# Kernel optimization log

Hardware: AMD Instinct MI355X
Metric: run time of the kernel (lower is better)

The kernel has to match this reference:

```python
import jax, jax.numpy as jnp
import numpy as np

MIN_NORM = 1e-15
BALL_EPS = 1e-5  # fp32 boundary eps used by hgcn PoincareBall.proj
C_IN = 1.0       # curvature = 1/r_in^2, r_in = 1.0
C_OUT = 1.0      # curvature = 1/r_out^2, r_out = 1.0


def _artanh(x):
    # hgcn clamps to +/-(1-1e-15); use 1e-7 so fp32 does not round to exactly 1
    x = jnp.clip(x, -1.0 + 1e-7, 1.0 - 1e-7)
    return 0.5 * (jnp.log1p(x) - jnp.log1p(-x))


def _norm(x):
    return jnp.maximum(jnp.linalg.norm(x, axis=-1, keepdims=True), MIN_NORM)


def proj(x, c):
    norm = _norm(x)
    maxnorm = (1.0 - BALL_EPS) / jnp.sqrt(c)
    return jnp.where(norm > maxnorm, x / norm * maxnorm, x)


def expmap0(u, c):
    sc = jnp.sqrt(c)
    un = _norm(u)
    return jnp.tanh(sc * un) * u / (sc * un)


def logmap0(p, c):
    sc = jnp.sqrt(c)
    pn = _norm(p)
    return _artanh(sc * pn) * p / (sc * pn)


def mobius_matvec(m, x, c):
    sc = jnp.sqrt(c)
    xn = _norm(x)
    mx = x @ m.T                      # [N, out]
    mxn = _norm(mx)
    res = jnp.tanh(mxn / xn * _artanh(sc * xn)) * mx / (mxn * sc)
    zero_row = jnp.all(mx == 0, axis=-1, keepdims=True)
    return jnp.where(zero_row, jnp.zeros((), dtype=res.dtype), res)


def mobius_add(x, y, c):
    x2 = jnp.sum(x * x, axis=-1, keepdims=True)
    y2 = jnp.sum(y * y, axis=-1, keepdims=True)
    xy = jnp.sum(x * y, axis=-1, keepdims=True)
    num = (1.0 + 2.0 * c * xy + c * y2) * x + (1.0 - c * x2) * y
    denom = 1.0 + 2.0 * c * xy + c * c * x2 * y2
    return num / jnp.maximum(denom, MIN_NORM)


def setup_inputs() -> dict:
    key = jax.random.key(0)
    k1, k2, k3, k4 = jax.random.split(key, 4)
    N, D_IN, D_OUT = 8192, 256, 256
    # points on the ball: small tangent vectors mapped through proj
    x = proj(0.05 * jax.random.normal(k1, (N, D_IN), dtype=jnp.float32), C_IN)
    # dense row-normalized adjacency
    adj = jax.random.uniform(k2, (N, N), dtype=jnp.float32)
    adj = adj / jnp.sum(adj, axis=1, keepdims=True)
    # xavier_uniform with gain sqrt(2)
    bound = np.sqrt(2.0) * np.sqrt(6.0 / (D_IN + D_OUT))
    weight = jax.random.uniform(k3, (D_OUT, D_IN), dtype=jnp.float32,
                                minval=-bound, maxval=bound)
    bias = 0.01 * jax.random.normal(k4, (D_OUT,), dtype=jnp.float32)
    return {"x": x, "adj": adj, "weight": weight, "bias": bias}


def reference(x, adj, weight, bias):
    # --- HypLinear (dropout=0 in eval) ---
    h = proj(mobius_matvec(weight, x, C_IN), C_IN)
    hyp_bias = proj(expmap0(bias[None, :], C_IN), C_IN)  # proj_tan0 = identity
    h = proj(mobius_add(h, hyp_bias, C_IN), C_IN)
    # --- HypAgg (use_att=False): aggregate in tangent space at origin ---
    x_tangent = logmap0(h, C_IN)
    support_t = adj @ x_tangent                          # [N, out]
    h = proj(expmap0(support_t, C_IN), C_IN)
    # --- HypAct: relu in tangent space, re-embed with c_out ---
    xt = jax.nn.relu(logmap0(h, C_IN))                   # proj_tan0 = identity
    return proj(expmap0(xt, C_OUT), C_OUT)
```

## Files before the change

kernel.cpp:

```cpp
#include <hip/hip_runtime.h>
#include <stdint.h>

#define DIM 256
#define NROWS 8192
#define KTOT 8192

typedef unsigned short u16;
typedef short bf16x8 __attribute__((ext_vector_type(8)));
typedef float f32x4 __attribute__((ext_vector_type(4)));

__device__ __forceinline__ u16 f2bf(float x) {
  uint32_t u = __float_as_uint(x);
  u = (u + 0x7FFFu + ((u >> 16) & 1u)) >> 16;
  return (u16)u;
}

__device__ __forceinline__ float wsum(float v) {
  v += __shfl_xor(v, 32, 64);
  v += __shfl_xor(v, 16, 64);
  v += __shfl_xor(v, 8, 64);
  v += __shfl_xor(v, 4, 64);
  v += __shfl_xor(v, 2, 64);
  v += __shfl_xor(v, 1, 64);
  return v;
}

__device__ __forceinline__ float artanh_c(float x) {
  const float lim = 1.0f - 1e-7f;
  x = fminf(fmaxf(x, -lim), lim);
  return 0.5f * (log1pf(x) - log1pf(-x));
}

__global__ __launch_bounds__(256)
void hgcn_k1(const float* __restrict__ x, const float* __restrict__ w,
             float* __restrict__ mx) {
  __shared__ float xs_t[32][64];
  __shared__ float ws_t[32][64];
  int t = threadIdx.x;
  int tx = t & 15, ty = t >> 4;
  int bi = blockIdx.x, bj = blockIdx.y;
  int lr = t >> 2, lc = (t & 3) * 8;
  const float* xp = x + (size_t)(bi * 64 + lr) * DIM + lc;
  const float* wp = w + (size_t)(bj * 64 + lr) * DIM + lc;
  float acc[4][4] = {};
  for (int kb = 0; kb < DIM; kb += 32) {
    float4 a0 = *(const float4*)(xp + kb);
    float4 a1 = *(const float4*)(xp + kb + 4);
    float4 b0 = *(const float4*)(wp + kb);
    float4 b1 = *(const float4*)(wp + kb + 4);
    __syncthreads();
    xs_t[lc + 0][lr] = a0.x; xs_t[lc + 1][lr] = a0.y;
    xs_t[lc + 2][lr] = a0.z; xs_t[lc + 3][lr] = a0.w;
    xs_t[lc + 4][lr] = a1.x; xs_t[lc + 5][lr] = a1.y;
    xs_t[lc + 6][lr] = a1.z; xs_t[lc + 7][lr] = a1.w;
    ws_t[lc + 0][lr] = b0.x; ws_t[lc + 1][lr] = b0.y;
    ws_t[lc + 2][lr] = b0.z; ws_t[lc + 3][lr] = b0.w;
    ws_t[lc + 4][lr] = b1.x; ws_t[lc + 5][lr] = b1.y;
    ws_t[lc + 6][lr] = b1.z; ws_t[lc + 7][lr] = b1.w;
    __syncthreads();
#pragma unroll
    for (int k = 0; k < 32; ++k) {
      float4 xv = *(const float4*)&xs_t[k][ty * 4];
      float4 wv = *(const float4*)&ws_t[k][tx * 4];
      float xr[4] = {xv.x, xv.y, xv.z, xv.w};
      float wr[4] = {wv.x, wv.y, wv.z, wv.w};
#pragma unroll
      for (int ii = 0; ii < 4; ++ii)
#pragma unroll
        for (int jj = 0; jj < 4; ++jj)
          acc[ii][jj] += xr[ii] * wr[jj];
    }
  }
#pragma unroll
  for (int ii = 0; ii < 4; ++ii) {
    float4 o = {acc[ii][0], acc[ii][1], acc[ii][2], acc[ii][3]};
    *(float4*)(mx + (size_t)(bi * 64 + ty * 4 + ii) * DIM + bj * 64 + tx * 4) = o;
  }
}

__global__ __launch_bounds__(256)
void hgcn_k2(const float* __restrict__ x, const float* __restrict__ mx,
             const float* __restrict__ bias, u16* __restrict__ xtT) {
  __shared__ u16 xl[64][256];
  const float maxn = 1.0f - 1e-5f;
  int t = threadIdx.x;
  int wave = t >> 6, lane = t & 63;
  int c0 = lane * 4;

  float4 b4 = *(const float4*)(bias + c0);
  float bn2 = wsum(b4.x * b4.x + b4.y * b4.y + b4.z * b4.z + b4.w * b4.w);
  float bn = fmaxf(sqrtf(bn2), 1e-15f);
  float sb = tanhf(bn) / bn;
  float hbx = b4.x * sb, hby = b4.y * sb, hbz = b4.z * sb, hbw = b4.w * sb;
  float ebn2 = wsum(hbx * hbx + hby * hby + hbz * hbz + hbw * hbw);
  float ebn = fmaxf(sqrtf(ebn2), 1e-15f);
  float sp = ebn > maxn ? maxn / ebn : 1.0f;
  hbx *= sp; hby *= sp; hbz *= sp; hbw *= sp;
  float y2 = (ebn * sp) * (ebn * sp);

  for (int rr = 0; rr < 16; ++rr) {
    int iloc = wave * 16 + rr;
    size_t row = (size_t)blockIdx.x * 64 + iloc;
    float4 xv = *(const float4*)(x + row * DIM + c0);
    float4 mv = *(const float4*)(mx + row * DIM + c0);
    float xn2 = wsum(xv.x * xv.x + xv.y * xv.y + xv.z * xv.z + xv.w * xv.w);
    float mxn2 = wsum(mv.x * mv.x + mv.y * mv.y + mv.z * mv.z + mv.w * mv.w);
    int zloc = (mv.x == 0.0f) && (mv.y == 0.0f) && (mv.z == 0.0f) && (mv.w == 0.0f);
    int zrow = __all(zloc);
    float xn = fmaxf(sqrtf(xn2), 1e-15f);
    float mxn = fmaxf(sqrtf(mxn2), 1e-15f);
    float rfac = tanhf(mxn / xn * artanh_c(xn)) / mxn;
    if (zrow) rfac = 0.0f;
    float hx = mv.x * rfac, hy = mv.y * rfac, hz = mv.z * rfac, hw = mv.w * rfac;
    float hn = fmaxf(fabsf(rfac) * mxn, 1e-15f);
    float s1 = hn > maxn ? maxn / hn : 1.0f;
    hx *= s1; hy *= s1; hz *= s1; hw *= s1;
    float x2 = (hn * s1) * (hn * s1);
    float xy = wsum(hx * hbx + hy * hby + hz * hbz + hw * hbw);
    float ca = 1.0f + 2.0f * xy + y2;
    float cb = 1.0f - x2;
    float den = 1.0f + 2.0f * xy + x2 * y2;
    float inv = 1.0f / fmaxf(den, 1e-15f);
    float ox = (ca * hx + cb * hbx) * inv;
    float oy = (ca * hy + cb * hby) * inv;
    float oz = (ca * hz + cb * hbz) * inv;
    float ow = (ca * hw + cb * hbw) * inv;
    float on2 = wsum(ox * ox + oy * oy + oz * oz + ow * ow);
    float on = fmaxf(sqrtf(on2), 1e-15f);
    float s2 = on > maxn ? maxn / on : 1.0f;
    ox *= s2; oy *= s2; oz *= s2; ow *= s2;
    float pn = fmaxf(on * s2, 1e-15f);
    float lf = artanh_c(pn) / pn;
    u16 tmp[4] = {f2bf(ox * lf), f2bf(oy * lf), f2bf(oz * lf), f2bf(ow * lf)};
    *(uint2*)&xl[iloc][c0] = *(const uint2*)tmp;
  }
  __syncthreads();
  int c = t;
  size_t ob = (size_t)c * KTOT + (size_t)blockIdx.x * 64;
  for (int ch = 0; ch < 8; ++ch) {
    u16 tmp[8];
#pragma unroll
    for (int q = 0; q < 8; ++q) tmp[q] = xl[ch * 8 + q][c];
    *(uint4*)(xtT + ob + ch * 8) = *(const uint4*)tmp;
  }
}

__global__ __launch_bounds__(256, 2)
void hgcn_k3(const float* __restrict__ adj, const u16* __restrict__ xtT,
             float* __restrict__ p0, float* __restrict__ p1) {
  __shared__ u16 ldsA[2][256 * 64];
  __shared__ u16 ldsB[2][32 * 64];
  int t = threadIdx.x;
  int wave = t >> 6, lane = t & 63;
  int l15 = lane & 15, l4 = lane >> 4;
  int m0 = blockIdx.x * 32;
  int kbase = blockIdx.y * (KTOT / 2);
  float* outp = blockIdx.y ? p1 : p0;
  int mloc = t >> 3;
  int chB = t & 7;

  f32x4 acc[4][2];
#pragma unroll
  for (int i = 0; i < 4; ++i)
#pragma unroll
    for (int j = 0; j < 2; ++j)
      acc[i][j] = (f32x4){0.f, 0.f, 0.f, 0.f};

  const int NSTEP = (KTOT / 2) / 64;

  {
    int kabs = kbase;
#pragma unroll
    for (int q = 0; q < 8; ++q) {
      int sb = (q * 4 + wave) * 64;
      int slot = sb + lane;
      int n = slot >> 3, ch = slot & 7;
      int sch = ch ^ (n & 7);
      const u16* src = xtT + (size_t)n * KTOT + kabs + sch * 8;
      __builtin_amdgcn_global_load_lds(
          (const __attribute__((address_space(1))) void*)src,
          (__attribute__((address_space(3))) void*)&ldsA[0][sb * 8], 16, 0, 0);
    }
    const float* ap = adj + (size_t)(m0 + mloc) * KTOT + kabs + chB * 8;
    float4 r0 = *(const float4*)ap;
    float4 r1 = *(const float4*)(ap + 4);
    u16 tmp[8] = {f2bf(r0.x), f2bf(r0.y), f2bf(r0.z), f2bf(r0.w),
                  f2bf(r1.x), f2bf(r1.y), f2bf(r1.z), f2bf(r1.w)};
    int pch = chB ^ (mloc & 7);
    *(uint4*)&ldsB[0][mloc * 64 + pch * 8] = *(const uint4*)tmp;
  }
  __syncthreads();

  for (int s = 0; s < NSTEP; ++s) {
    int cur = s & 1, nb = cur ^ 1;
    float4 r0, r1;
    bool more = (s + 1 < NSTEP);
    if (more) {
      int kabs = kbase + (s + 1) * 64;
#pragma unroll
      for (int q = 0; q < 8; ++q) {
        int sb = (q * 4 + wave) * 64;
        int slot = sb + lane;
        int n = slot >> 3, ch = slot & 7;
        int sch = ch ^ (n & 7);
        const u16* src = xtT + (size_t)n * KTOT + kabs + sch * 8;
        __builtin_amdgcn_global_load_lds(
            (const __attribute__((address_space(1))) void*)src,
            (__attribute__((address_space(3))) void*)&ldsA[nb][sb * 8], 16, 0, 0);
      }
      const float* ap = adj + (size_t)(m0 + mloc) * KTOT + kabs + chB * 8;
      r0 = *(const float4*)ap;
      r1 = *(const float4*)(ap + 4);
    }
#pragma unroll
    for (int kc = 0; kc < 2; ++kc) {
      bf16x8 bfr[2];
#pragma unroll
      for (int mi = 0; mi < 2; ++mi) {
        int r = mi * 16 + l15;
        int ch = (kc * 4 + l4) ^ (r & 7);
        bfr[mi] = *(const bf16x8*)&ldsB[cur][r * 64 + ch * 8];
      }
#pragma unroll
      for (int ni = 0; ni < 4; ++ni) {
        int rn = wave * 64 + ni * 16 + l15;
        int ch = (kc * 4 + l4) ^ (rn & 7);
        bf16x8 afr = *(const bf16x8*)&ldsA[cur][rn * 64 + ch * 8];
        acc[ni][0] = __builtin_amdgcn_mfma_f32_16x16x32_bf16(afr, bfr[0], acc[ni][0], 0, 0, 0);
        acc[ni][1] = __builtin_amdgcn_mfma_f32_16x16x32_bf16(afr, bfr[1], acc[ni][1], 0, 0, 0);
      }
    }
    if (more) {
      u16 tmp[8] = {f2bf(r0.x), f2bf(r0.y), f2bf(r0.z), f2bf(r0.w),
                    f2bf(r1.x), f2bf(r1.y), f2bf(r1.z), f2bf(r1.w)};
      int pch = chB ^ (mloc & 7);
      *(uint4*)&ldsB[nb][mloc * 64 + pch * 8] = *(const uint4*)tmp;
    }
    __syncthreads();
  }

#pragma unroll
  for (int ni = 0; ni < 4; ++ni)
#pragma unroll
    for (int mi = 0; mi < 2; ++mi) {
      int n = wave * 64 + ni * 16 + l4 * 4;
      int m = m0 + mi * 16 + l15;
      *(f32x4*)(outp + (size_t)m * DIM + n) = acc[ni][mi];
    }
}

__global__ __launch_bounds__(256)
void hgcn_k4(const float* __restrict__ p0, const float* __restrict__ p1,
             float* __restrict__ out) {
  const float maxn = 1.0f - 1e-5f;
  int t = threadIdx.x;
  int wave = t >> 6, lane = t & 63;
  size_t row = (size_t)blockIdx.x * 4 + wave;
  int c0 = lane * 4;
  float4 a = *(const float4*)(p0 + row * DIM + c0);
  float4 b = *(const float4*)(p1 + row * DIM + c0);
  float sx = a.x + b.x, sy = a.y + b.y, sz = a.z + b.z, sw = a.w + b.w;
  float un2 = wsum(sx * sx + sy * sy + sz * sz + sw * sw);
  float un = fmaxf(sqrtf(un2), 1e-15f);
  float t1 = tanhf(un) / un;
  float hx = sx * t1, hy = sy * t1, hz = sz * t1, hw = sw * t1;
  float hn = fmaxf(fabsf(t1) * un, 1e-15f);
  float s1 = hn > maxn ? maxn / hn : 1.0f;
  hx *= s1; hy *= s1; hz *= s1; hw *= s1;
  float pn = fmaxf(hn * s1, 1e-15f);
  float lf = artanh_c(pn) / pn;
  float rx = fmaxf(hx * lf, 0.0f), ry = fmaxf(hy * lf, 0.0f);
  float rz = fmaxf(hz * lf, 0.0f), rw = fmaxf(hw * lf, 0.0f);
  float rn2 = wsum(rx * rx + ry * ry + rz * rz + rw * rw);
  float rn = fmaxf(sqrtf(rn2), 1e-15f);
  float t2 = tanhf(rn) / rn;
  float ox = rx * t2, oy = ry * t2, oz = rz * t2, ow = rw * t2;
  float on = fmaxf(fabsf(t2) * rn, 1e-15f);
  float s3 = on > maxn ? maxn / on : 1.0f;
  float4 o = {ox * s3, oy * s3, oz * s3, ow * s3};
  *(float4*)(out + row * DIM + c0) = o;
}

extern "C" void kernel_launch(void* const* d_in, const int* in_sizes, int n_in,
                              void* d_out, int out_size, void* d_ws, size_t ws_size,
                              hipStream_t stream) {
  const float* x = (const float*)d_in[0];
  const float* adj = (const float*)d_in[1];
  const float* wgt = (const float*)d_in[2];
  const float* bias = (const float*)d_in[3];
  float* out = (float*)d_out;
  char* ws = (char*)d_ws;
  float* mx = (float*)ws;
  u16* xtT = (u16*)(ws + (8u << 20));
  float* p1 = (float*)(ws + (12u << 20));
  float* p0 = mx;

  hipLaunchKernelGGL(hgcn_k1, dim3(128, 4), dim3(256), 0, stream, x, wgt, mx);
  hipLaunchKernelGGL(hgcn_k2, dim3(128), dim3(256), 0, stream, x, mx, bias, xtT);
  hipLaunchKernelGGL(hgcn_k3, dim3(256, 2), dim3(256), 0, stream, adj, xtT, p0, p1);
  hipLaunchKernelGGL(hgcn_k4, dim3(2048), dim3(256), 0, stream, p0, p1, out);
}
```

Baseline: 190.9 us.

## Restructure aggregation GEMM with 3-stage pipeline, 512-thread blocks and XCD-aware tiling

```diff
diff --git a/kernel.cpp b/kernel.cpp
--- a/kernel.cpp
+++ b/kernel.cpp
@@ -145,19 +145,94 @@
   }
 }
 
-__global__ __launch_bounds__(256, 2)
+#define A_TILE (256 * 64)
+#define B_TILE (64 * 64)
+
+__device__ __forceinline__ void k3_issueA(const u16* __restrict__ xtT, u16* __restrict__ dstbase,
+                                          int kabs, int wave, int lane) {
+#pragma unroll
+  for (int q = 0; q < 4; ++q) {
+    int sb = (q * 8 + wave) * 64;
+    int slot = sb + lane;
+    int n = slot >> 3;
+    int sch = (slot & 7) ^ (n & 7);
+    __builtin_amdgcn_global_load_lds(
+        (const __attribute__((address_space(1))) void*)(xtT + (size_t)n * KTOT + kabs + sch * 8),
+        (__attribute__((address_space(3))) void*)(dstbase + sb * 8), 16, 0, 0);
+  }
+}
+
+__device__ __forceinline__ void k3_writeB(u16* __restrict__ bbuf, int rowB, int chB,
+                                          const float4& ra, const float4& rb) {
+  u16 tmp[8] = {f2bf(ra.x), f2bf(ra.y), f2bf(ra.z), f2bf(ra.w),
+                f2bf(rb.x), f2bf(rb.y), f2bf(rb.z), f2bf(rb.w)};
+  *(uint4*)&bbuf[rowB * 64 + (chB ^ (rowB & 7)) * 8] = *(const uint4*)tmp;
+}
+
+__device__ __forceinline__ void k3_compute(const u16* __restrict__ ba, const u16* __restrict__ bb,
+                                           f32x4 (&acc)[4][2], int wm, int wn, int l15, int l4) {
+  __builtin_amdgcn_s_setprio(1);
+#pragma unroll
+  for (int kc = 0; kc < 2; ++kc) {
+    bf16x8 bfr[2];
+#pragma unroll
+    for (int mi = 0; mi < 2; ++mi) {
+      int r = wm * 32 + mi * 16 + l15;
+      int ch = (kc * 4 + l4) ^ (r & 7);
+      bfr[mi] = *(const bf16x8*)&bb[r * 64 + ch * 8];
+    }
+#pragma unroll
+    for (int ni = 0; ni < 4; ++ni) {
+      int rn = wn * 64 + ni * 16 + l15;
+      int ch = (kc * 4 + l4) ^ (rn & 7);
+      bf16x8 afr = *(const bf16x8*)&ba[rn * 64 + ch * 8];
+      acc[ni][0] = __builtin_amdgcn_mfma_f32_16x16x32_bf16(afr, bfr[0], acc[ni][0], 0, 0, 0);
+      acc[ni][1] = __builtin_amdgcn_mfma_f32_16x16x32_bf16(afr, bfr[1], acc[ni][1], 0, 0, 0);
+    }
+  }
+  __builtin_amdgcn_s_setprio(0);
+}
+
+#define K3_WAITV(N) { asm volatile("s_waitcnt vmcnt(" #N ")" ::: "memory"); __builtin_amdgcn_sched_barrier(0); }
+#define K3_LGKM0    { asm volatile("s_waitcnt lgkmcnt(0)" ::: "memory"); __builtin_amdgcn_sched_barrier(0); }
+
+#define K3_BODY(S, RCA, RCB, RIA, RIB, DOISSUE)                                        \
+  {                                                                                    \
+    K3_WAITV(4);             \
+    k3_writeB(ldsB + (((S) + 1) % 3) * B_TILE, rowB, chB, RCA, RCB);                   \
+    K3_LGKM0;                                                                          \
+    __builtin_amdgcn_s_barrier();                  \
+    if (DOISSUE) {                                                                     \
+      const float* ap = adjp + ((S) + 2) * 64;                                         \
+      RIA = *(const float4*)ap;                                                        \
+      RIB = *(const float4*)(ap + 4);                                                  \
+      __builtin_amdgcn_sched_barrier(0);                                               \
+      k3_issueA(xtT, ldsA + (((S) + 2) % 3) * A_TILE, kbase + ((S) + 2) * 64, wave, lane); \
+      __builtin_amdgcn_sched_barrier(0);                                               \
+    }                                                                                  \
+    k3_compute(ldsA + ((S) % 3) * A_TILE, ldsB + ((S) % 3) * B_TILE, acc, wm, wn, l15, l4); \
+  }
+
+__global__ __launch_bounds__(512, 2)
 void hgcn_k3(const float* __restrict__ adj, const u16* __restrict__ xtT,
              float* __restrict__ p0, float* __restrict__ p1) {
-  __shared__ u16 ldsA[2][256 * 64];
-  __shared__ u16 ldsB[2][32 * 64];
+  __shared__ u16 ldsA[3 * A_TILE];
+  __shared__ u16 ldsB[3 * B_TILE];
   int t = threadIdx.x;
   int wave = t >> 6, lane = t & 63;
   int l15 = lane & 15, l4 = lane >> 4;
-  int m0 = blockIdx.x * 32;
-  int kbase = blockIdx.y * (KTOT / 2);
-  float* outp = blockIdx.y ? p1 : p0;
-  int mloc = t >> 3;
-  int chB = t & 7;
+  int wm = wave >> 2, wn = wave & 3;
+
+  int bid = blockIdx.x;
+  int xcd = bid & 7;
+  int y = xcd >> 2;
+  int m_tile = (bid >> 3) * 4 + (xcd & 3);
+  int m0 = m_tile * 64;
+  int kbase = y * (KTOT / 2);
+  float* outp = y ? p1 : p0;
+
+  int rowB = t >> 3, chB = t & 7;
+  const float* adjp = adj + (size_t)(m0 + rowB) * KTOT + kbase + chB * 8;
 
   f32x4 acc[4][2];
 #pragma unroll
@@ -166,85 +241,35 @@
     for (int j = 0; j < 2; ++j)
       acc[i][j] = (f32x4){0.f, 0.f, 0.f, 0.f};
 
-  const int NSTEP = (KTOT / 2) / 64;
-
-  {
-    int kabs = kbase;
-#pragma unroll
-    for (int q = 0; q < 8; ++q) {
-      int sb = (q * 4 + wave) * 64;
-      int slot = sb + lane;
-      int n = slot >> 3, ch = slot & 7;
-      int sch = ch ^ (n & 7);
-      const u16* src = xtT + (size_t)n * KTOT + kabs + sch * 8;
-      __builtin_amdgcn_global_load_lds(
-          (const __attribute__((address_space(1))) void*)src,
-          (__attribute__((address_space(3))) void*)&ldsA[0][sb * 8], 16, 0, 0);
-    }
-    const float* ap = adj + (size_t)(m0 + mloc) * KTOT + kabs + chB * 8;
-    float4 r0 = *(const float4*)ap;
-    float4 r1 = *(const float4*)(ap + 4);
-    u16 tmp[8] = {f2bf(r0.x), f2bf(r0.y), f2bf(r0.z), f2bf(r0.w),
-                  f2bf(r1.x), f2bf(r1.y), f2bf(r1.z), f2bf(r1.w)};
-    int pch = chB ^ (mloc & 7);
-    *(uint4*)&ldsB[0][mloc * 64 + pch * 8] = *(const uint4*)tmp;
-  }
-  __syncthreads();
-
-  for (int s = 0; s < NSTEP; ++s) {
-    int cur = s & 1, nb = cur ^ 1;
-    float4 r0, r1;
-    bool more = (s + 1 < NSTEP);
-    if (more) {
-      int kabs = kbase + (s + 1) * 64;
-#pragma unroll
-      for (int q = 0; q < 8; ++q) {
-        int sb = (q * 4 + wave) * 64;
-        int slot = sb + lane;
-        int n = slot >> 3, ch = slot & 7;
-        int sch = ch ^ (n & 7);
-        const u16* src = xtT + (size_t)n * KTOT + kabs + sch * 8;
-        __builtin_amdgcn_global_load_lds(
-            (const __attribute__((address_space(1))) void*)src,
-            (__attribute__((address_space(3))) void*)&ldsA[nb][sb * 8], 16, 0, 0);
-      }
-      const float* ap = adj + (size_t)(m0 + mloc) * KTOT + kabs + chB * 8;
-      r0 = *(const float4*)ap;
-      r1 = *(const float4*)(ap + 4);
-    }
-#pragma unroll
-    for (int kc = 0; kc < 2; ++kc) {
-      bf16x8 bfr[2];
-#pragma unroll
-      for (int mi = 0; mi < 2; ++mi) {
-        int r = mi * 16 + l15;
-        int ch = (kc * 4 + l4) ^ (r & 7);
-        bfr[mi] = *(const bf16x8*)&ldsB[cur][r * 64 + ch * 8];
-      }
-#pragma unroll
-      for (int ni = 0; ni < 4; ++ni) {
-        int rn = wave * 64 + ni * 16 + l15;
-        int ch = (kc * 4 + l4) ^ (rn & 7);
-        bf16x8 afr = *(const bf16x8*)&ldsA[cur][rn * 64 + ch * 8];
-        acc[ni][0] = __builtin_amdgcn_mfma_f32_16x16x32_bf16(afr, bfr[0], acc[ni][0], 0, 0, 0);
-        acc[ni][1] = __builtin_amdgcn_mfma_f32_16x16x32_bf16(afr, bfr[1], acc[ni][1], 0, 0, 0);
-      }
-    }
-    if (more) {
-      u16 tmp[8] = {f2bf(r0.x), f2bf(r0.y), f2bf(r0.z), f2bf(r0.w),
-                    f2bf(r1.x), f2bf(r1.y), f2bf(r1.z), f2bf(r1.w)};
-      int pch = chB ^ (mloc & 7);
-      *(uint4*)&ldsB[nb][mloc * 64 + pch * 8] = *(const uint4*)tmp;
-    }
-    __syncthreads();
-  }
+  float4 r0a, r0b, r1a, r1b;
+  r0a = *(const float4*)adjp;
+  r0b = *(const float4*)(adjp + 4);
+  __builtin_amdgcn_sched_barrier(0);
+  k3_issueA(xtT, ldsA, kbase, wave, lane);
+  __builtin_amdgcn_sched_barrier(0);
+  r1a = *(const float4*)(adjp + 64);
+  r1b = *(const float4*)(adjp + 64 + 4);
+  __builtin_amdgcn_sched_barrier(0);
+  k3_issueA(xtT, ldsA + A_TILE, kbase + 64, wave, lane);
+  __builtin_amdgcn_sched_barrier(0);
+  K3_WAITV(10);
+  k3_writeB(ldsB, rowB, chB, r0a, r0b);
+
+  for (int s = 0; s < 62; s += 2) {
+    K3_BODY(s, r1a, r1b, r0a, r0b, true);
+    K3_BODY(s + 1, r0a, r0b, r1a, r1b, true);
+  }
+  K3_BODY(62, r1a, r1b, r0a, r0b, false);
+  K3_WAITV(0);
+  __builtin_amdgcn_s_barrier();
+  k3_compute(ldsA + (63 % 3) * A_TILE, ldsB + (63 % 3) * B_TILE, acc, wm, wn, l15, l4);
 
 #pragma unroll
   for (int ni = 0; ni < 4; ++ni)
 #pragma unroll
     for (int mi = 0; mi < 2; ++mi) {
-      int n = wave * 64 + ni * 16 + l4 * 4;
-      int m = m0 + mi * 16 + l15;
+      int n = wn * 64 + ni * 16 + l4 * 4;
+      int m = m0 + wm * 32 + mi * 16 + l15;
       *(f32x4*)(outp + (size_t)m * DIM + n) = acc[ni][mi];
     }
 }
@@ -297,6 +322,6 @@
 
   hipLaunchKernelGGL(hgcn_k1, dim3(128, 4), dim3(256), 0, stream, x, wgt, mx);
   hipLaunchKernelGGL(hgcn_k2, dim3(128), dim3(256), 0, stream, x, mx, bias, xtT);
-  hipLaunchKernelGGL(hgcn_k3, dim3(256, 2), dim3(256), 0, stream, adj, xtT, p0, p1);
+  hipLaunchKernelGGL(hgcn_k3, dim3(256), dim3(512), 0, stream, adj, xtT, p0, p1);
   hipLaunchKernelGGL(hgcn_k4, dim3(2048), dim3(256), 0, stream, p0, p1, out);
 }
```

Measured after the change: 172.8 us. 9.5% less time.

## Replace LDS-staged adj GEMM with direct-register MFMA tiles and wider split-K

Applied to the files above, without the earlier changes.

```diff
diff --git a/kernel.cpp b/kernel.cpp
--- a/kernel.cpp
+++ b/kernel.cpp
@@ -145,121 +145,91 @@
   }
 }
 
-__global__ __launch_bounds__(256, 2)
+__global__ __launch_bounds__(256, 4)
 void hgcn_k3(const float* __restrict__ adj, const u16* __restrict__ xtT,
-             float* __restrict__ p0, float* __restrict__ p1) {
-  __shared__ u16 ldsA[2][256 * 64];
-  __shared__ u16 ldsB[2][32 * 64];
+             float* __restrict__ pbase, int xps_log, int ksize) {
   int t = threadIdx.x;
   int wave = t >> 6, lane = t & 63;
   int l15 = lane & 15, l4 = lane >> 4;
-  int m0 = blockIdx.x * 32;
-  int kbase = blockIdx.y * (KTOT / 2);
-  float* outp = blockIdx.y ? p1 : p0;
-  int mloc = t >> 3;
-  int chB = t & 7;
-
-  f32x4 acc[4][2];
+  int wm = wave >> 1, wn = wave & 1;
+  int bid = blockIdx.x;
+  int xps_m1 = (1 << xps_log) - 1;
+  int split = (bid & 7) >> xps_log;
+  int sub = (bid & 7) & xps_m1;
+  int tt = ((bid >> 3) << xps_log) + sub;
+  int m_tile = tt >> 1, nb = tt & 1;
+  int m0 = m_tile * 128 + wm * 64;
+  int n0 = nb * 128 + wn * 64;
+  int kbase = split * ksize;
+  float* outp = pbase + (size_t)split * ((size_t)NROWS * DIM);
+
+  const u16* ap[4];
+  const float* bp[4];
+#pragma unroll
+  for (int ni = 0; ni < 4; ++ni)
+    ap[ni] = xtT + (size_t)(n0 + ni * 16 + l15) * KTOT + kbase + l4 * 8;
+#pragma unroll
+  for (int mi = 0; mi < 4; ++mi)
+    bp[mi] = adj + (size_t)(m0 + mi * 16 + l15) * KTOT + kbase + l4 * 8;
+
+  f32x4 acc[4][4];
 #pragma unroll
   for (int i = 0; i < 4; ++i)
 #pragma unroll
-    for (int j = 0; j < 2; ++j)
+    for (int j = 0; j < 4; ++j)
       acc[i][j] = (f32x4){0.f, 0.f, 0.f, 0.f};
 
-  const int NSTEP = (KTOT / 2) / 64;
-
-  {
-    int kabs = kbase;
-#pragma unroll
-    for (int q = 0; q < 8; ++q) {
-      int sb = (q * 4 + wave) * 64;
-      int slot = sb + lane;
-      int n = slot >> 3, ch = slot & 7;
-      int sch = ch ^ (n & 7);
-      const u16* src = xtT + (size_t)n * KTOT + kabs + sch * 8;
-      __builtin_amdgcn_global_load_lds(
-          (const __attribute__((address_space(1))) void*)src,
-          (__attribute__((address_space(3))) void*)&ldsA[0][sb * 8], 16, 0, 0);
+#pragma unroll 2
+  for (int kk = 0; kk < ksize; kk += 32) {
+    bf16x8 a[4], b[4];
+#pragma unroll
+    for (int ni = 0; ni < 4; ++ni)
+      a[ni] = *(const bf16x8*)(ap[ni] + kk);
+#pragma unroll
+    for (int mi = 0; mi < 4; ++mi) {
+      const float* p = bp[mi] + kk;
+      float4 f0 = ((const float4*)p)[0];
+      float4 f1 = ((const float4*)p)[1];
+      uint32_t w0, w1, w2, w3;
+      asm("v_cvt_pk_bf16_f32 %0, %1, %2" : "=v"(w0) : "v"(f0.x), "v"(f0.y));
+      asm("v_cvt_pk_bf16_f32 %0, %1, %2" : "=v"(w1) : "v"(f0.z), "v"(f0.w));
+      asm("v_cvt_pk_bf16_f32 %0, %1, %2" : "=v"(w2) : "v"(f1.x), "v"(f1.y));
+      asm("v_cvt_pk_bf16_f32 %0, %1, %2" : "=v"(w3) : "v"(f1.z), "v"(f1.w));
+      union { uint32_t u[4]; bf16x8 v; } cv;
+      cv.u[0] = w0; cv.u[1] = w1; cv.u[2] = w2; cv.u[3] = w3;
+      b[mi] = cv.v;
     }
-    const float* ap = adj + (size_t)(m0 + mloc) * KTOT + kabs + chB * 8;
-    float4 r0 = *(const float4*)ap;
-    float4 r1 = *(const float4*)(ap + 4);
-    u16 tmp[8] = {f2bf(r0.x), f2bf(r0.y), f2bf(r0.z), f2bf(r0.w),
-                  f2bf(r1.x), f2bf(r1.y), f2bf(r1.z), f2bf(r1.w)};
-    int pch = chB ^ (mloc & 7);
-    *(uint4*)&ldsB[0][mloc * 64 + pch * 8] = *(const uint4*)tmp;
-  }
-  __syncthreads();
-
-  for (int s = 0; s < NSTEP; ++s) {
-    int cur = s & 1, nb = cur ^ 1;
-    float4 r0, r1;
-    bool more = (s + 1 < NSTEP);
-    if (more) {
-      int kabs = kbase + (s + 1) * 64;
-#pragma unroll
-      for (int q = 0; q < 8; ++q) {
-        int sb = (q * 4 + wave) * 64;
-        int slot = sb + lane;
-        int n = slot >> 3, ch = slot & 7;
-        int sch = ch ^ (n & 7);
-        const u16* src = xtT + (size_t)n * KTOT + kabs + sch * 8;
-        __builtin_amdgcn_global_load_lds(
-            (const __attribute__((address_space(1))) void*)src,
-            (__attribute__((address_space(3))) void*)&ldsA[nb][sb * 8], 16, 0, 0);
-      }
-      const float* ap = adj + (size_t)(m0 + mloc) * KTOT + kabs + chB * 8;
-      r0 = *(const float4*)ap;
-      r1 = *(const float4*)(ap + 4);
-    }
-#pragma unroll
-    for (int kc = 0; kc < 2; ++kc) {
-      bf16x8 bfr[2];
-#pragma unroll
-      for (int mi = 0; mi < 2; ++mi) {
-        int r = mi * 16 + l15;
-        int ch = (kc * 4 + l4) ^ (r & 7);
-        bfr[mi] = *(const bf16x8*)&ldsB[cur][r * 64 + ch * 8];
-      }
-#pragma unroll
-      for (int ni = 0; ni < 4; ++ni) {
-        int rn = wave * 64 + ni * 16 + l15;
-        int ch = (kc * 4 + l4) ^ (rn & 7);
-        bf16x8 afr = *(const bf16x8*)&ldsA[cur][rn * 64 + ch * 8];
-        acc[ni][0] = __builtin_amdgcn_mfma_f32_16x16x32_bf16(afr, bfr[0], acc[ni][0], 0, 0, 0);
-        acc[ni][1] = __builtin_amdgcn_mfma_f32_16x16x32_bf16(afr, bfr[1], acc[ni][1], 0, 0, 0);
-      }
-    }
-    if (more) {
-      u16 tmp[8] = {f2bf(r0.x), f2bf(r0.y), f2bf(r0.z), f2bf(r0.w),
-                    f2bf(r1.x), f2bf(r1.y), f2bf(r1.z), f2bf(r1.w)};
-      int pch = chB ^ (mloc & 7);
-      *(uint4*)&ldsB[nb][mloc * 64 + pch * 8] = *(const uint4*)tmp;
-    }
-    __syncthreads();
+#pragma unroll
+    for (int ni = 0; ni < 4; ++ni)
+#pragma unroll
+      for (int mi = 0; mi < 4; ++mi)
+        acc[ni][mi] = __builtin_amdgcn_mfma_f32_16x16x32_bf16(a[ni], b[mi], acc[ni][mi], 0, 0, 0);
   }
 
 #pragma unroll
   for (int ni = 0; ni < 4; ++ni)
 #pragma unroll
-    for (int mi = 0; mi < 2; ++mi) {
-      int n = wave * 64 + ni * 16 + l4 * 4;
+    for (int mi = 0; mi < 4; ++mi) {
+      int n = n0 + ni * 16 + l4 * 4;
       int m = m0 + mi * 16 + l15;
       *(f32x4*)(outp + (size_t)m * DIM + n) = acc[ni][mi];
     }
 }
 
 __global__ __launch_bounds__(256)
-void hgcn_k4(const float* __restrict__ p0, const float* __restrict__ p1,
+void hgcn_k4(const float* __restrict__ pbase, size_t pstride, int nsplit,
              float* __restrict__ out) {
   const float maxn = 1.0f - 1e-5f;
   int t = threadIdx.x;
   int wave = t >> 6, lane = t & 63;
   size_t row = (size_t)blockIdx.x * 4 + wave;
   int c0 = lane * 4;
-  float4 a = *(const float4*)(p0 + row * DIM + c0);
-  float4 b = *(const float4*)(p1 + row * DIM + c0);
-  float sx = a.x + b.x, sy = a.y + b.y, sz = a.z + b.z, sw = a.w + b.w;
+  size_t off = row * DIM + c0;
+  float sx = 0.f, sy = 0.f, sz = 0.f, sw = 0.f;
+  for (int i = 0; i < nsplit; ++i) {
+    float4 v = *(const float4*)(pbase + (size_t)i * pstride + off);
+    sx += v.x; sy += v.y; sz += v.z; sw += v.w;
+  }
   float un2 = wsum(sx * sx + sy * sy + sz * sz + sw * sw);
   float un = fmaxf(sqrtf(un2), 1e-15f);
   float t1 = tanhf(un) / un;
@@ -278,7 +248,7 @@
   float on = fmaxf(fabsf(t2) * rn, 1e-15f);
   float s3 = on > maxn ? maxn / on : 1.0f;
   float4 o = {ox * s3, oy * s3, oz * s3, ow * s3};
-  *(float4*)(out + row * DIM + c0) = o;
+  *(float4*)(out + off) = o;
 }
 
 extern "C" void kernel_launch(void* const* d_in, const int* in_sizes, int n_in,
@@ -292,11 +262,19 @@
   char* ws = (char*)d_ws;
   float* mx = (float*)ws;
   u16* xtT = (u16*)(ws + (8u << 20));
-  float* p1 = (float*)(ws + (12u << 20));
-  float* p0 = mx;
+  float* pbase = (float*)(ws + (12u << 20));
+
+  const size_t PBYTES = (size_t)NROWS * DIM * 4;
+  const size_t BASE = (size_t)12 << 20;
+  int ksplit = (ws_size >= BASE + 8 * PBYTES) ? 8
+             : (ws_size >= BASE + 4 * PBYTES) ? 4 : 2;
+  int xps_log = (ksplit == 8) ? 0 : (ksplit == 4) ? 1 : 2;
+  int ksize = KTOT / ksplit;
 
   hipLaunchKernelGGL(hgcn_k1, dim3(128, 4), dim3(256), 0, stream, x, wgt, mx);
   hipLaunchKernelGGL(hgcn_k2, dim3(128), dim3(256), 0, stream, x, mx, bias, xtT);
-  hipLaunchKernelGGL(hgcn_k3, dim3(256, 2), dim3(256), 0, stream, adj, xtT, p0, p1);
-  hipLaunchKernelGGL(hgcn_k4, dim3(2048), dim3(256), 0, stream, p0, p1, out);
-}
+  hipLaunchKernelGGL(hgcn_k3, dim3(128 * ksplit), dim3(256), 0, stream,
+                     adj, xtT, pbase, xps_log, ksize);
+  hipLaunchKernelGGL(hgcn_k4, dim3(2048), dim3(256), 0, stream,
+                     pbase, (size_t)NROWS * DIM, ksplit, out);
+}
```

Result: slower. 263.8 us (+38.2%).
